# Performance work log

Measured on AMD Instinct MI355X. Metric: run time of the kernel, lower is better.

## Reference

```python
import jax, jax.numpy as jnp
import numpy as np

B, T, D, U = 32, 4096, 512, 256

def setup_inputs() -> dict:
    key = jax.random.key(0)
    ks = jax.random.split(key, 5)
    s = 1.0 / np.sqrt(D)
    return {
        "values": jax.random.normal(ks[0], (B, T, D), dtype=jnp.float32),
        "query": jax.random.normal(ks[1], (B, D), dtype=jnp.float32),
        "W1": jax.random.normal(ks[2], (D, U), dtype=jnp.float32) * s,
        "b1": jnp.zeros((U,), dtype=jnp.float32),
        "W2": jax.random.normal(ks[3], (D, U), dtype=jnp.float32) * s,
        "b2": jnp.zeros((U,), dtype=jnp.float32),
        "V": jax.random.normal(ks[4], (U, 1), dtype=jnp.float32) * (1.0 / np.sqrt(U)),
        "bV": jnp.zeros((1,), dtype=jnp.float32),
    }

def reference(values, query, W1, b1, W2, b2, V, bV):
    # values: [B,T,D], query: [B,D]
    h_vals = jnp.einsum('btd,du->btu', values, W1) + b1          # [B,T,U]
    h_query = (query @ W2 + b2)[:, None, :]                       # [B,1,U]
    score = jnp.einsum('btu,uo->bto', jnp.tanh(h_vals + h_query), V) + bV  # [B,T,1]
    attention_weights = jax.nn.softmax(score, axis=1)             # [B,T,1]
    context_vector = jnp.sum(attention_weights * values, axis=1)  # [B,D]
    return context_vector, attention_weights
```

## Files before the change

### kernel.cpp

```cpp
#include <hip/hip_runtime.h>
#include <math.h>
#include <stdint.h>

#define BB 32
#define TT 4096
#define DD 512
#define UU 256

#define KC 32
#define NKC (DD/KC)
#define LDB 40
#define TC 256

typedef __attribute__((ext_vector_type(8))) short short8;
typedef __attribute__((ext_vector_type(8))) unsigned short ushort8;
typedef __attribute__((ext_vector_type(4))) float floatx4;

typedef const __attribute__((address_space(1))) unsigned int GU32;
typedef __attribute__((address_space(3))) unsigned int LU32;

__device__ __forceinline__ unsigned short bf16_rne(float x) {
  union { float f; uint32_t u; } v; v.f = x;
  uint32_t r = v.u + 0x7FFFu + ((v.u >> 16) & 1u);
  return (unsigned short)(r >> 16);
}
__device__ __forceinline__ float tanh_fast(float x) {
  float e = __expf(2.0f * x);
  return 1.0f - 2.0f * __builtin_amdgcn_rcpf(e + 1.0f);
}

__global__ __launch_bounds__(256) void prep_w1_kernel(
    const float* __restrict__ W1, unsigned short* __restrict__ staged) {
  const int kc = blockIdx.x;
  const int u = threadIdx.x;
  __attribute__((aligned(16))) unsigned short row[LDB];
#pragma unroll
  for (int kk = 0; kk < KC; ++kk)
    row[kk] = bf16_rne(W1[(kc * KC + kk) * UU + u]);
#pragma unroll
  for (int kk = KC; kk < LDB; ++kk) row[kk] = 0;
  unsigned short* dst = staged + ((size_t)kc * UU + u) * LDB;
#pragma unroll
  for (int i = 0; i < 5; ++i) ((uint4*)dst)[i] = *(const uint4*)&row[i * 8];
}

__global__ __launch_bounds__(256) void hquery_kernel(
    const float* __restrict__ query, const float* __restrict__ W2,
    const float* __restrict__ b2, const float* __restrict__ b1,
    float* __restrict__ hq) {
  const int b = blockIdx.x;
  const int u = threadIdx.x;
  __shared__ float qs[DD];
  for (int d = threadIdx.x; d < DD; d += 256) qs[d] = query[b * DD + d];
  __syncthreads();
  float acc = b2[u] + b1[u];
  for (int d = 0; d < DD; ++d) acc += qs[d] * W2[d * UU + u];
  hq[b * UU + u] = acc;
}

__global__ __launch_bounds__(256) void score_kernel(
    const float* __restrict__ values, const unsigned short* __restrict__ w1s,
    const float* __restrict__ hq, const float* __restrict__ V,
    const float* __restrict__ bV, float* __restrict__ scores) {
  const int b = blockIdx.y;
  const int t0 = blockIdx.x * 64;
  const int tid = threadIdx.x;
  const int wave = tid >> 6;
  const int lane = tid & 63;
  const int c = lane & 15;
  const int q = lane >> 4;

  __shared__ unsigned short As[64 * LDB];
  __shared__ unsigned short Bs[UU * LDB];
  __shared__ float redW[4][64];

  floatx4 acc[4][4];
#pragma unroll
  for (int ti = 0; ti < 4; ++ti)
#pragma unroll
    for (int ui = 0; ui < 4; ++ui) acc[ti][ui] = (floatx4){0.f, 0.f, 0.f, 0.f};

  const int ar = tid >> 2;
  const int aseg = tid & 3;
  const float* asrc =
      values + ((size_t)b * TT + t0) * DD + (size_t)ar * DD + aseg * 8;

  float4 a0 = *(const float4*)asrc;
  float4 a1 = *(const float4*)(asrc + 4);

  for (int kc = 0; kc < NKC; ++kc) {
    __syncthreads();
    {
      ushort8 t8;
      t8[0] = bf16_rne(a0.x); t8[1] = bf16_rne(a0.y);
      t8[2] = bf16_rne(a0.z); t8[3] = bf16_rne(a0.w);
      t8[4] = bf16_rne(a1.x); t8[5] = bf16_rne(a1.y);
      t8[6] = bf16_rne(a1.z); t8[7] = bf16_rne(a1.w);
      *(ushort8*)&As[ar * LDB + aseg * 8] = t8;
    }
    {
      GU32* src = (GU32*)(w1s + (size_t)kc * UU * LDB);
      LU32* dst = (LU32*)Bs;
#pragma unroll
      for (int i = 0; i < 5; ++i)
        __builtin_amdgcn_global_load_lds(src + (i * 256 + tid) * 4,
                                         dst + (i * 256 + tid) * 4, 16, 0, 0);
    }
    __syncthreads();

    short8 afr[4], bfr[4];
#pragma unroll
    for (int ti = 0; ti < 4; ++ti)
      afr[ti] = *(const short8*)&As[(ti * 16 + c) * LDB + q * 8];
#pragma unroll
    for (int ui = 0; ui < 4; ++ui)
      bfr[ui] = *(const short8*)&Bs[(wave * 64 + ui * 16 + c) * LDB + q * 8];
#pragma unroll
    for (int ti = 0; ti < 4; ++ti)
#pragma unroll
      for (int ui = 0; ui < 4; ++ui)
        acc[ti][ui] = __builtin_amdgcn_mfma_f32_16x16x32_bf16(
            afr[ti], bfr[ui], acc[ti][ui], 0, 0, 0);

    if (kc + 1 < NKC) {
      a0 = *(const float4*)(asrc + (kc + 1) * KC);
      a1 = *(const float4*)(asrc + (kc + 1) * KC + 4);
    }
  }

  float hqv[4], vv[4];
#pragma unroll
  for (int ui = 0; ui < 4; ++ui) {
    const int u = wave * 64 + ui * 16 + c;
    hqv[ui] = hq[b * UU + u];
    vv[ui] = V[u];
  }
#pragma unroll
  for (int ti = 0; ti < 4; ++ti)
#pragma unroll
    for (int r = 0; r < 4; ++r) {
      float e = 0.0f;
#pragma unroll
      for (int ui = 0; ui < 4; ++ui)
        e += tanh_fast(acc[ti][ui][r] + hqv[ui]) * vv[ui];
      e += __shfl_xor(e, 1, 64);
      e += __shfl_xor(e, 2, 64);
      e += __shfl_xor(e, 4, 64);
      e += __shfl_xor(e, 8, 64);
      if (c == 0) redW[wave][ti * 16 + q * 4 + r] = e;
    }
  __syncthreads();
  if (tid < 64) {
    const float s =
        bV[0] + redW[0][tid] + redW[1][tid] + redW[2][tid] + redW[3][tid];
    scores[b * TT + t0 + tid] = s;
  }
}

__global__ __launch_bounds__(256) void softmax_stats_kernel(
    const float* __restrict__ scores, float* __restrict__ stats) {
  const int b = blockIdx.x;
  const int tid = threadIdx.x;
  __shared__ float sm[256];
  float m = -1e30f;
  for (int t = tid; t < TT; t += 256) m = fmaxf(m, scores[b * TT + t]);
  sm[tid] = m;
  __syncthreads();
  for (int s = 128; s > 0; s >>= 1) {
    if (tid < s) sm[tid] = fmaxf(sm[tid], sm[tid + s]);
    __syncthreads();
  }
  m = sm[0];
  __syncthreads();
  float l = 0.0f;
  for (int t = tid; t < TT; t += 256) l += __expf(scores[b * TT + t] - m);
  sm[tid] = l;
  __syncthreads();
  for (int s = 128; s > 0; s >>= 1) {
    if (tid < s) sm[tid] += sm[tid + s];
    __syncthreads();
  }
  if (tid == 0) {
    stats[2 * b] = m;
    stats[2 * b + 1] = sm[0];
  }
}

__global__ __launch_bounds__(256) void context_kernel(
    const float* __restrict__ values, const float* __restrict__ scores,
    const float* __restrict__ stats, float* __restrict__ out) {
  const int b = blockIdx.y;
  const int tc0 = blockIdx.x * TC;
  const int tid = threadIdx.x;
  const float m = stats[2 * b];
  const float linv = 1.0f / stats[2 * b + 1];

  __shared__ float wts[TC];
  {
    const float w = __expf(scores[b * TT + tc0 + tid] - m) * linv;
    wts[tid] = w;
    out[BB * DD + b * TT + tc0 + tid] = w;
  }
  __syncthreads();

  const int sub = tid >> 7;
  const int d4 = tid & 127;
  const float4* vp = (const float4*)(values + ((size_t)b * TT + tc0) * DD);
  float4 acc = {0.f, 0.f, 0.f, 0.f};
#pragma unroll 4
  for (int t = sub; t < TC; t += 2) {
    const float w = wts[t];
    const float4 v = vp[(size_t)t * (DD / 4) + d4];
    acc.x += w * v.x; acc.y += w * v.y; acc.z += w * v.z; acc.w += w * v.w;
  }
  float* o = out + b * DD + d4 * 4;
  atomicAdd(o + 0, acc.x);
  atomicAdd(o + 1, acc.y);
  atomicAdd(o + 2, acc.z);
  atomicAdd(o + 3, acc.w);
}

extern "C" void kernel_launch(void* const* d_in, const int* in_sizes, int n_in,
                              void* d_out, int out_size, void* d_ws, size_t ws_size,
                              hipStream_t stream) {
  const float* values = (const float*)d_in[0];
  const float* query  = (const float*)d_in[1];
  const float* W1     = (const float*)d_in[2];
  const float* b1     = (const float*)d_in[3];
  const float* W2     = (const float*)d_in[4];
  const float* b2     = (const float*)d_in[5];
  const float* V      = (const float*)d_in[6];
  const float* bV     = (const float*)d_in[7];
  float* out = (float*)d_out;

  float* ws = (float*)d_ws;
  float* hq     = ws;
  float* scores = ws + BB * UU;
  float* stats  = scores + BB * TT;
  unsigned short* w1s = (unsigned short*)(stats + 2 * BB);

  hipMemsetAsync(out, 0, BB * DD * sizeof(float), stream);

  prep_w1_kernel<<<NKC, 256, 0, stream>>>(W1, w1s);
  hquery_kernel<<<BB, 256, 0, stream>>>(query, W2, b2, b1, hq);
  score_kernel<<<dim3(TT / 64, BB), 256, 0, stream>>>(values, w1s, hq, V, bV, scores);
  softmax_stats_kernel<<<BB, 256, 0, stream>>>(scores, stats);
  context_kernel<<<dim3(TT / TC, BB), 256, 0, stream>>>(values, scores, stats, out);
}
```

Measured before the change: 464.0 us.

## Fuse softmax partials and weighted context into score kernel with flash-style combine

The score kernel now computes each 64-row tile's local max, exp-sum and exp-weighted partial context while its values tile is likely still in cache. A small combine kernel merges the per-tile partials with online-softmax rescaling, and a light kernel writes the normalized attention weights. This removes the separate full second pass over values (256MB) and the atomics and memset. In exchange it writes per-tile partial context to the workspace and adds an epilogue to the score kernel. The reread of the 128KB tile in that epilogue may hit L2 or MALL.

```diff
diff --git a/kernel.cpp b/kernel.cpp
--- a/kernel.cpp
+++ b/kernel.cpp
@@ -10,7 +10,7 @@
 #define KC 32
 #define NKC (DD/KC)
 #define LDB 40
-#define TC 256
+#define NTILE (TT/64)
 
 typedef __attribute__((ext_vector_type(8))) short short8;
 typedef __attribute__((ext_vector_type(8))) unsigned short ushort8;
@@ -61,9 +61,11 @@
 __global__ __launch_bounds__(256) void score_kernel(
     const float* __restrict__ values, const unsigned short* __restrict__ w1s,
     const float* __restrict__ hq, const float* __restrict__ V,
-    const float* __restrict__ bV, float* __restrict__ scores) {
+    const float* __restrict__ bV, float* __restrict__ scores,
+    float* __restrict__ pml, float* __restrict__ pctx) {
   const int b = blockIdx.y;
-  const int t0 = blockIdx.x * 64;
+  const int blk = blockIdx.x;
+  const int t0 = blk * 64;
   const int tid = threadIdx.x;
   const int wave = tid >> 6;
   const int lane = tid & 63;
@@ -73,6 +75,7 @@
   __shared__ unsigned short As[64 * LDB];
   __shared__ unsigned short Bs[UU * LDB];
   __shared__ float redW[4][64];
+  __shared__ float warr[64];
 
   floatx4 acc[4][4];
 #pragma unroll
@@ -154,70 +157,78 @@
     const float s =
         bV[0] + redW[0][tid] + redW[1][tid] + redW[2][tid] + redW[3][tid];
     scores[b * TT + t0 + tid] = s;
-  }
-}
-
-__global__ __launch_bounds__(256) void softmax_stats_kernel(
-    const float* __restrict__ scores, float* __restrict__ stats) {
+    redW[0][tid] = s;
+  }
+  __syncthreads();
+  float mb = -1e30f;
+#pragma unroll 8
+  for (int t = 0; t < 64; ++t) mb = fmaxf(mb, redW[0][t]);
+  if (tid < 64) warr[tid] = __expf(redW[0][tid] - mb);
+  __syncthreads();
+  float lb = 0.0f;
+#pragma unroll 8
+  for (int t = 0; t < 64; ++t) lb += warr[t];
+
+  const float2* vp = (const float2*)(values + ((size_t)b * TT + t0) * DD);
+  float2 c2 = {0.f, 0.f};
+#pragma unroll 4
+  for (int t = 0; t < 64; ++t) {
+    const float w = warr[t];
+    const float2 v = vp[(size_t)t * (DD / 2) + tid];
+    c2.x += w * v.x;
+    c2.y += w * v.y;
+  }
+  *(float2*)&pctx[((size_t)b * NTILE + blk) * DD + 2 * tid] = c2;
+  if (tid == 0) {
+    pml[(b * NTILE + blk) * 2 + 0] = mb;
+    pml[(b * NTILE + blk) * 2 + 1] = lb;
+  }
+}
+
+__global__ __launch_bounds__(256) void combine_kernel(
+    const float* __restrict__ pml, const float* __restrict__ pctx,
+    float* __restrict__ out, float* __restrict__ stats) {
   const int b = blockIdx.x;
   const int tid = threadIdx.x;
-  __shared__ float sm[256];
+  __shared__ float mls[2 * NTILE];
+  __shared__ float cs[NTILE];
+  if (tid < 2 * NTILE) mls[tid] = pml[b * 2 * NTILE + tid];
+  __syncthreads();
   float m = -1e30f;
-  for (int t = tid; t < TT; t += 256) m = fmaxf(m, scores[b * TT + t]);
-  sm[tid] = m;
-  __syncthreads();
-  for (int s = 128; s > 0; s >>= 1) {
-    if (tid < s) sm[tid] = fmaxf(sm[tid], sm[tid + s]);
-    __syncthreads();
-  }
-  m = sm[0];
+#pragma unroll 8
+  for (int i = 0; i < NTILE; ++i) m = fmaxf(m, mls[2 * i]);
+  if (tid < NTILE) cs[tid] = __expf(mls[2 * tid] - m);
   __syncthreads();
   float l = 0.0f;
-  for (int t = tid; t < TT; t += 256) l += __expf(scores[b * TT + t] - m);
-  sm[tid] = l;
-  __syncthreads();
-  for (int s = 128; s > 0; s >>= 1) {
-    if (tid < s) sm[tid] += sm[tid + s];
-    __syncthreads();
-  }
+#pragma unroll 8
+  for (int i = 0; i < NTILE; ++i) l += cs[i] * mls[2 * i + 1];
+
+  const float2* pp = (const float2*)(pctx + (size_t)b * NTILE * DD);
+  float2 acc = {0.f, 0.f};
+#pragma unroll 4
+  for (int i = 0; i < NTILE; ++i) {
+    const float cw = cs[i];
+    const float2 p = pp[(size_t)i * (DD / 2) + tid];
+    acc.x += cw * p.x;
+    acc.y += cw * p.y;
+  }
+  const float linv = 1.0f / l;
+  out[b * DD + 2 * tid + 0] = acc.x * linv;
+  out[b * DD + 2 * tid + 1] = acc.y * linv;
   if (tid == 0) {
-    stats[2 * b] = m;
-    stats[2 * b + 1] = sm[0];
-  }
-}
-
-__global__ __launch_bounds__(256) void context_kernel(
-    const float* __restrict__ values, const float* __restrict__ scores,
-    const float* __restrict__ stats, float* __restrict__ out) {
+    stats[2 * b + 0] = m;
+    stats[2 * b + 1] = l;
+  }
+}
+
+__global__ __launch_bounds__(256) void weights_kernel(
+    const float* __restrict__ scores, const float* __restrict__ stats,
+    float* __restrict__ out) {
   const int b = blockIdx.y;
-  const int tc0 = blockIdx.x * TC;
-  const int tid = threadIdx.x;
+  const int t = blockIdx.x * 256 + threadIdx.x;
   const float m = stats[2 * b];
   const float linv = 1.0f / stats[2 * b + 1];
-
-  __shared__ float wts[TC];
-  {
-    const float w = __expf(scores[b * TT + tc0 + tid] - m) * linv;
-    wts[tid] = w;
-    out[BB * DD + b * TT + tc0 + tid] = w;
-  }
-  __syncthreads();
-
-  const int sub = tid >> 7;
-  const int d4 = tid & 127;
-  const float4* vp = (const float4*)(values + ((size_t)b * TT + tc0) * DD);
-  float4 acc = {0.f, 0.f, 0.f, 0.f};
-#pragma unroll 4
-  for (int t = sub; t < TC; t += 2) {
-    const float w = wts[t];
-    const float4 v = vp[(size_t)t * (DD / 4) + d4];
-    acc.x += w * v.x; acc.y += w * v.y; acc.z += w * v.z; acc.w += w * v.w;
-  }
-  float* o = out + b * DD + d4 * 4;
-  atomicAdd(o + 0, acc.x);
-  atomicAdd(o + 1, acc.y);
-  atomicAdd(o + 2, acc.z);
-  atomicAdd(o + 3, acc.w);
+  out[BB * DD + b * TT + t] = __expf(scores[b * TT + t] - m) * linv;
 }
 
 extern "C" void kernel_launch(void* const* d_in, const int* in_sizes, int n_in,
@@ -237,13 +248,14 @@
   float* hq     = ws;
   float* scores = ws + BB * UU;
   float* stats  = scores + BB * TT;
-  unsigned short* w1s = (unsigned short*)(stats + 2 * BB);
-
-  hipMemsetAsync(out, 0, BB * DD * sizeof(float), stream);
+  float* pml    = stats + 2 * BB;
+  float* pctx   = pml + BB * NTILE * 2;
+  unsigned short* w1s = (unsigned short*)(pctx + (size_t)BB * NTILE * DD);
 
   prep_w1_kernel<<<NKC, 256, 0, stream>>>(W1, w1s);
   hquery_kernel<<<BB, 256, 0, stream>>>(query, W2, b2, b1, hq);
-  score_kernel<<<dim3(TT / 64, BB), 256, 0, stream>>>(values, w1s, hq, V, bV, scores);
-  softmax_stats_kernel<<<BB, 256, 0, stream>>>(scores, stats);
-  context_kernel<<<dim3(TT / TC, BB), 256, 0, stream>>>(values, scores, stats, out);
-}
+  score_kernel<<<dim3(NTILE, BB), 256, 0, stream>>>(
+      values, w1s, hq, V, bV, scores, pml, pctx);
+  combine_kernel<<<BB, 256, 0, stream>>>(pml, pctx, out, stats);
+  weights_kernel<<<dim3(TT / 256, BB), 256, 0, stream>>>(scores, stats, out);
+}
```

Result: no change. 461.7 us (-0.5%).
